# Optimization experiments

Measured on AMD Instinct MI355X. Metric: run time of the kernel, lower is better.

The kernel has to match this reference:

```python
import jax, jax.numpy as jnp
import numpy as np

B, T, H = 2, 1024, 4096
HK, HV, DK, DV = 8, 32, 64, 64
VPK = HV // HK            # value heads per key head = 4
KEY_DIM = HK * DK         # 512
VAL_DIM = HV * DV         # 2048
CONV_DIM = 2 * KEY_DIM + VAL_DIM  # 3072
KSZ = 4
EPS = 1e-5
L2_EPS = 1e-6


def _l2norm(x):
    return x * jax.lax.rsqrt(jnp.sum(x * x, axis=-1, keepdims=True) + L2_EPS)


def setup_inputs() -> dict:
    key = jax.random.key(0)
    ks = jax.random.split(key, 8)
    s = 0.02
    return {
        "hidden_states": jax.random.normal(ks[0], (B, T, H), jnp.float32),
        "W_qkvz": jax.random.normal(ks[1], (H, 2 * KEY_DIM + 2 * VAL_DIM), jnp.float32) * s,
        "W_ba": jax.random.normal(ks[2], (H, 2 * HV), jnp.float32) * s,
        "conv_w": jax.random.normal(ks[3], (CONV_DIM, KSZ), jnp.float32) * 0.1,
        "dt_bias": jnp.ones((HV,), jnp.float32),
        "A_log": jnp.log(jax.random.uniform(ks[4], (HV,), jnp.float32, 1.0, 16.0)),
        "norm_w": jnp.ones((DV,), jnp.float32),
        "W_out": jax.random.normal(ks[5], (VAL_DIM, H), jnp.float32) * s,
    }


def _forward(hidden_states, W_qkvz, W_ba, conv_w, dt_bias, A_log, norm_w, W_out):
    # --- projections ---
    qkvz = hidden_states @ W_qkvz                       # [B,T,5120]
    ba = hidden_states @ W_ba                           # [B,T,64]
    # fix_query_key_value_ordering: per key head [q(Dk), k(Dk), v(vpk*Dv), z(vpk*Dv)]
    qkvz = qkvz.reshape(B, T, HK, 2 * DK + 2 * VPK * DV)
    q = qkvz[..., :DK]                                  # [B,T,HK,DK]
    k = qkvz[..., DK:2 * DK]
    v = qkvz[..., 2 * DK:2 * DK + VPK * DV].reshape(B, T, HV, DV)
    z = qkvz[..., 2 * DK + VPK * DV:].reshape(B, T, HV, DV)
    ba = ba.reshape(B, T, HK, 2 * VPK)
    b = ba[..., :VPK].reshape(B, T, HV)
    a = ba[..., VPK:].reshape(B, T, HV)

    # --- causal depthwise conv over concatenated qkv, then silu ---
    mixed = jnp.concatenate(
        [q.reshape(B, T, KEY_DIM), k.reshape(B, T, KEY_DIM), v.reshape(B, T, VAL_DIM)], axis=-1)
    padded = jnp.pad(mixed, ((0, 0), (KSZ - 1, 0), (0, 0)))
    conv = sum(padded[:, j:j + T, :] * conv_w[:, j] for j in range(KSZ))
    conv = jax.nn.silu(conv)
    q = conv[..., :KEY_DIM].reshape(B, T, HK, DK)
    k = conv[..., KEY_DIM:2 * KEY_DIM].reshape(B, T, HK, DK)
    v = conv[..., 2 * KEY_DIM:].reshape(B, T, HV, DV)

    # --- fused GDN gating: g = -exp(A_log)*softplus(a+dt_bias), beta = sigmoid(b) ---
    g = -jnp.exp(A_log) * jax.nn.softplus(a + dt_bias)  # [B,T,HV]
    beta = jax.nn.sigmoid(b)                            # [B,T,HV]

    # --- q/k l2 norm + scale, broadcast key heads to value heads ---
    q = _l2norm(q) * (DK ** -0.5)
    k = _l2norm(k)
    q = jnp.repeat(q, VPK, axis=2)                      # [B,T,HV,DK]
    k = jnp.repeat(k, VPK, axis=2)

    # --- gated delta-rule recurrence over time ---
    def step(S, inp):
        qt, kt, vt, gt, bt = inp                        # qt/kt [B,HV,DK], vt [B,HV,DV]
        S = S * jnp.exp(gt)[..., None, None]            # decay
        pred = jnp.einsum('bhk,bhkv->bhv', kt, S)
        delta = (vt - pred) * bt[..., None]
        S = S + jnp.einsum('bhk,bhv->bhkv', kt, delta)
        o = jnp.einsum('bhk,bhkv->bhv', qt, S)
        return S, o

    xs = (q.transpose(1, 0, 2, 3), k.transpose(1, 0, 2, 3), v.transpose(1, 0, 2, 3),
          g.transpose(1, 0, 2), beta.transpose(1, 0, 2))
    S0 = jnp.zeros((B, HV, DK, DV), q.dtype)
    _, o = jax.lax.scan(step, S0, xs)                   # [T,B,HV,DV]
    o = o.transpose(1, 0, 2, 3)                         # [B,T,HV,DV]

    # --- gated RMSNorm (norm before gate) + out projection ---
    o_n = o * jax.lax.rsqrt(jnp.mean(o * o, axis=-1, keepdims=True) + EPS) * norm_w
    o_n = o_n * jax.nn.silu(z)
    return o_n.reshape(B, T, VAL_DIM) @ W_out           # [B,T,H]


def reference(hidden_states, W_qkvz, W_ba, conv_w, dt_bias, A_log, norm_w, W_out):
    return _forward(hidden_states, W_qkvz, W_ba, conv_w, dt_bias, A_log, norm_w, W_out)
```

## Files before the change

kernel.cpp:

```cpp
#include <hip/hip_runtime.h>
#include <hip/hip_bf16.h>
#include <cstdint>
#include <cstddef>


typedef __attribute__((ext_vector_type(8))) short short8;
typedef __attribute__((ext_vector_type(4))) float f32x4;

__device__ __forceinline__ short f2bf(float f) {
  union { float f; unsigned u; } x; x.f = f;
  unsigned r = x.u + 0x7fffu + ((x.u >> 16) & 1u);
  return (short)(r >> 16);
}

__device__ __forceinline__ void gl_lds16(const short* g, short* l) {
  __builtin_amdgcn_global_load_lds(
      (const __attribute__((address_space(1))) void*)g,
      (__attribute__((address_space(3))) void*)l, 16, 0, 0);
}

__global__ __launch_bounds__(256) void to_bf16_kernel(const float* __restrict__ x,
                                                      short* __restrict__ y) {
  int i = blockIdx.x * 256 + threadIdx.x;
  float4 v = ((const float4*)x)[i];
  ushort4 r;
  r.x = (unsigned short)f2bf(v.x);
  r.y = (unsigned short)f2bf(v.y);
  r.z = (unsigned short)f2bf(v.z);
  r.w = (unsigned short)f2bf(v.w);
  ((ushort4*)y)[i] = r;
}

__global__ __launch_bounds__(256) void transpose_w1(const float* __restrict__ Wq,
                                                    const float* __restrict__ Wba,
                                                    short* __restrict__ Wt) {
  __shared__ float tile[32][33];
  int n0 = blockIdx.x * 32;
  int k0 = blockIdx.y * 32;
  int t = threadIdx.x;
  int r = t >> 5;
  int c = t & 31;
#pragma unroll
  for (int i = 0; i < 4; ++i) {
    int kl = r + i * 8;
    int n = n0 + c;
    float v = 0.f;
    if (n < 5120) v = Wq[(size_t)(k0 + kl) * 5120 + n];
    else if (n < 5184) v = Wba[(size_t)(k0 + kl) * 64 + (n - 5120)];
    tile[kl][c] = v;
  }
  __syncthreads();
#pragma unroll
  for (int i = 0; i < 4; ++i) {
    int nl = r + i * 8;
    int kl = c;
    Wt[(size_t)(n0 + nl) * 4096 + k0 + kl] = f2bf(tile[kl][nl]);
  }
}

__global__ __launch_bounds__(256) void transpose_w2(const float* __restrict__ W,
                                                    short* __restrict__ Wt) {
  __shared__ float tile[32][33];
  int n0 = blockIdx.x * 32;
  int k0 = blockIdx.y * 32;
  int t = threadIdx.x;
  int r = t >> 5;
  int c = t & 31;
#pragma unroll
  for (int i = 0; i < 4; ++i) {
    int kl = r + i * 8;
    tile[kl][c] = W[(size_t)(k0 + kl) * 4096 + n0 + c];
  }
  __syncthreads();
#pragma unroll
  for (int i = 0; i < 4; ++i) {
    int nl = r + i * 8;
    int kl = c;
    Wt[(size_t)(n0 + nl) * 2048 + k0 + kl] = f2bf(tile[kl][nl]);
  }
}

template <bool GUARD_N>
__global__ __launch_bounds__(256) void gemm128p(const short* __restrict__ A,
                                                const short* __restrict__ Bt,
                                                float* __restrict__ C,
                                                int N, int K, int MT) {
  __shared__ __align__(16) short As[3 * 4096];
  __shared__ __align__(16) short Bs[3 * 4096];
  const int tid = threadIdx.x;
  const int w = tid >> 6, lane = tid & 63;
  const int wm = w >> 1, wn = w & 1;

  const int nwg = gridDim.x;
  const int bid = blockIdx.x;
  const int swz = (bid & 7) * (nwg >> 3) + (bid >> 3);
  const int m0 = (swz % MT) * 128;
  const int n0 = (swz / MT) * 128;

  const int p0 = w * 64 + lane;
  const int rp0 = p0 >> 3, q0 = p0 & 7;
  const int mm0 = q0 ^ (rp0 & 7);
  const int srow = rp0 * 2 + (mm0 >> 2);
  const int scol = (mm0 & 3) << 3;
  const short* Ag = A + (size_t)(m0 + srow) * K + scol;
  const short* Bg = Bt + (size_t)(n0 + srow) * K + scol;
  const size_t rstep = (size_t)64 * K;

  const int fr = lane & 15;
  const int s = lane >> 4;
  int aoff[4], boff[4];
#pragma unroll
  for (int i = 0; i < 4; ++i) {
    int row = wm * 64 + i * 16 + fr;
    int rp = row >> 1;
    int q = (((row & 1) << 2) | s) ^ (rp & 7);
    aoff[i] = (rp * 8 + q) * 8;
  }
#pragma unroll
  for (int j = 0; j < 4; ++j) {
    int row = wn * 64 + j * 16 + fr;
    int rp = row >> 1;
    int q = (((row & 1) << 2) | s) ^ (rp & 7);
    boff[j] = (rp * 8 + q) * 8;
  }

  f32x4 acc[4][4];
#pragma unroll
  for (int i = 0; i < 4; ++i)
#pragma unroll
    for (int j = 0; j < 4; ++j) acc[i][j] = (f32x4){0.f, 0.f, 0.f, 0.f};

  const int NKT = K >> 5;

#define STAGE_A(kt, bb)                                                \
  { const short* g = Ag + (size_t)(kt) * 32;                           \
    gl_lds16(g,         &As[(bb) * 4096 + w * 512]);                   \
    gl_lds16(g + rstep, &As[(bb) * 4096 + 2048 + w * 512]); }
#define STAGE_B(kt, bb)                                                \
  { const short* g = Bg + (size_t)(kt) * 32;                           \
    gl_lds16(g,         &Bs[(bb) * 4096 + w * 512]);                   \
    gl_lds16(g + rstep, &Bs[(bb) * 4096 + 2048 + w * 512]); }

  STAGE_A(0, 0); STAGE_B(0, 0);
  STAGE_A(1, 1); STAGE_B(1, 1);
  asm volatile("s_waitcnt vmcnt(4)" ::: "memory");
  __builtin_amdgcn_s_barrier();
  __builtin_amdgcn_sched_barrier(0);

  int bi = 0;
  for (int kt = 0; kt < NKT; ++kt) {
    int bi2 = bi - 1; if (bi2 < 0) bi2 = 2;
    const short* Ab = &As[bi * 4096];
    const short* Bb = &Bs[bi * 4096];
    short8 af[2], bf[4];
#pragma unroll
    for (int i = 0; i < 2; ++i) af[i] = *(const short8*)&Ab[aoff[i]];
#pragma unroll
    for (int j = 0; j < 4; ++j) bf[j] = *(const short8*)&Bb[boff[j]];
    if (kt + 2 < NKT) STAGE_A(kt + 2, bi2);
    __builtin_amdgcn_s_barrier();
    asm volatile("s_waitcnt lgkmcnt(0)" ::: "memory");
    __builtin_amdgcn_sched_barrier(0);
    __builtin_amdgcn_s_setprio(1);
#pragma unroll
    for (int i = 0; i < 2; ++i)
#pragma unroll
      for (int j = 0; j < 4; ++j)
        acc[i][j] = __builtin_amdgcn_mfma_f32_16x16x32_bf16(af[i], bf[j], acc[i][j], 0, 0, 0);
    __builtin_amdgcn_s_setprio(0);
    __builtin_amdgcn_sched_barrier(0);
#pragma unroll
    for (int i = 0; i < 2; ++i) af[i] = *(const short8*)&Ab[aoff[i + 2]];
    if (kt + 2 < NKT) STAGE_B(kt + 2, bi2);
    if (kt < NKT - 2) { asm volatile("s_waitcnt vmcnt(4)" ::: "memory"); }
    else              { asm volatile("s_waitcnt vmcnt(0)" ::: "memory"); }
    __builtin_amdgcn_s_barrier();
    asm volatile("s_waitcnt lgkmcnt(0)" ::: "memory");
    __builtin_amdgcn_sched_barrier(0);
    __builtin_amdgcn_s_setprio(1);
#pragma unroll
    for (int i = 0; i < 2; ++i)
#pragma unroll
      for (int j = 0; j < 4; ++j)
        acc[i + 2][j] = __builtin_amdgcn_mfma_f32_16x16x32_bf16(af[i], bf[j], acc[i + 2][j], 0, 0, 0);
    __builtin_amdgcn_s_setprio(0);
    __builtin_amdgcn_sched_barrier(0);
    __builtin_amdgcn_s_barrier();
    ++bi; if (bi == 3) bi = 0;
  }
#undef STAGE_A
#undef STAGE_B

  const int rbase = (lane >> 4) << 2;
#pragma unroll
  for (int i = 0; i < 4; ++i) {
#pragma unroll
    for (int j = 0; j < 4; ++j) {
      int col = n0 + wn * 64 + j * 16 + fr;
      if (GUARD_N && col >= N) continue;
      int row = m0 + wm * 64 + i * 16 + rbase;
#pragma unroll
      for (int r = 0; r < 4; ++r)
        C[(size_t)(row + r) * N + col] = acc[i][j][r];
    }
  }
}

__global__ __launch_bounds__(256) void conv_kernel(const float* __restrict__ qkvz,
                                                   const float* __restrict__ conv_w,
                                                   float* __restrict__ mix) {
  __shared__ float sq[1024];
  __shared__ float scale[16];
  int bt = blockIdx.x;
  int t = bt & 1023;
  int tid = threadIdx.x;
  for (int c = tid; c < 3072; c += 256) {
    int col;
    if (c < 512) {
      col = (c >> 6) * 640 + (c & 63);
    } else if (c < 1024) {
      int c2 = c - 512;
      col = (c2 >> 6) * 640 + 64 + (c2 & 63);
    } else {
      int c3 = c - 1024;
      int hv = c3 >> 6;
      col = (hv >> 2) * 640 + 128 + (hv & 3) * 64 + (c3 & 63);
    }
    float acc = 0.f;
#pragma unroll
    for (int j = 0; j < 4; ++j) {
      int tt = t - 3 + j;
      if (tt >= 0) acc += qkvz[(size_t)(bt - 3 + j) * 5184 + col] * conv_w[c * 4 + j];
    }
    float sv = acc / (1.f + __expf(-acc));
    if (c < 1024)
      sq[c] = sv;
    else
      mix[(size_t)bt * 3072 + c] = sv;
  }
  __syncthreads();
  int g = tid >> 4, l = tid & 15;
  float p = 0.f;
#pragma unroll
  for (int i = 0; i < 4; ++i) {
    float v = sq[g * 64 + l * 4 + i];
    p += v * v;
  }
  p += __shfl_xor(p, 1);
  p += __shfl_xor(p, 2);
  p += __shfl_xor(p, 4);
  p += __shfl_xor(p, 8);
  if (l == 0) scale[g] = rsqrtf(p + 1e-6f);
  __syncthreads();
  for (int c = tid; c < 1024; c += 256) {
    float s = scale[c >> 6] * ((c < 512) ? 0.125f : 1.f);
    mix[(size_t)bt * 3072 + c] = sq[c] * s;
  }
}

__global__ __launch_bounds__(256) void gate_kernel(const float* __restrict__ qkvz,
                                                   const float* __restrict__ dt_bias,
                                                   const float* __restrict__ A_log,
                                                   float* __restrict__ gb,
                                                   float* __restrict__ beta) {
  int i = blockIdx.x * 256 + threadIdx.x;
  int hv = i & 31;
  int bt = i >> 5;
  int hk = hv >> 2, vp = hv & 3;
  const float* row = qkvz + (size_t)bt * 5184 + 5120 + hk * 8;
  float bv = row[vp];
  float av = row[4 + vp];
  float x = av + dt_bias[hv];
  float sp = (x > 20.f) ? x : log1pf(expf(x));
  gb[i] = -expf(A_log[hv]) * sp;
  beta[i] = 1.f / (1.f + expf(-bv));
}

__global__ __launch_bounds__(256) void precompute_kernel(
    const float* __restrict__ mix, const float* __restrict__ gbuf,
    const float* __restrict__ betab, float* __restrict__ Wbuf,
    float* __restrict__ Pbuf, float* __restrict__ Rbuf, float* __restrict__ cbuf) {
  __shared__ float Kt[64][68];
  __shared__ float Vb[64][68];
  __shared__ float AM[64][68];
  __shared__ float Mm[64][68];
  __shared__ float Tb[16][17];
  __shared__ float cs[64], bb[64];

  const int u = blockIdx.x;
  const int chunk = u & 15, hv = (u >> 4) & 31, b = u >> 9;
  const int hk = hv >> 2;
  const int t0g = b * 1024 + chunk * 64;
  const int tid = threadIdx.x;
  const int tr = tid >> 2, q4 = tid & 3;

  {
    const float* mrow = mix + (size_t)(t0g + tr) * 3072;
#pragma unroll
    for (int e = 0; e < 4; ++e) {
      int c0 = q4 * 16 + e * 4;
      float4 kv = *(const float4*)(mrow + 512 + hk * 64 + c0);
      Kt[c0 + 0][tr] = kv.x; Kt[c0 + 1][tr] = kv.y;
      Kt[c0 + 2][tr] = kv.z; Kt[c0 + 3][tr] = kv.w;
      *(float4*)&Vb[tr][c0] = *(const float4*)(mrow + 1024 + hv * 64 + c0);
    }
  }
  if (tid < 64) {
    cs[tid] = gbuf[(size_t)(t0g + tid) * 32 + hv];
    bb[tid] = betab[(size_t)(t0g + tid) * 32 + hv];
  }
  __syncthreads();
  for (int off = 1; off < 64; off <<= 1) {
    float v = 0.f;
    if (tid < 64 && tid >= off) v = cs[tid - off];
    __syncthreads();
    if (tid < 64) cs[tid] += v;
    __syncthreads();
  }
  if (tid < 64) cbuf[(size_t)u * 64 + tid] = cs[tid];

  {
    float acc[16];
#pragma unroll
    for (int i = 0; i < 16; ++i) acc[i] = 0.f;
    for (int d = 0; d < 64; ++d) {
      float kv = Kt[d][tr];
#pragma unroll
      for (int e = 0; e < 4; ++e) {
        float4 ks = *(const float4*)&Kt[d][q4 * 16 + e * 4];
        acc[e * 4 + 0] += kv * ks.x; acc[e * 4 + 1] += kv * ks.y;
        acc[e * 4 + 2] += kv * ks.z; acc[e * 4 + 3] += kv * ks.w;
      }
    }
    float bt_ = bb[tr], ct_ = cs[tr];
#pragma unroll
    for (int j = 0; j < 16; ++j) {
      int s = q4 * 16 + j;
      AM[tr][s] = (s < tr) ? bt_ * acc[j] * __expf(ct_ - cs[s]) : 0.f;
    }
  }
  __syncthreads();

  for (int i = tid; i < 64 * 68; i += 256) (&Mm[0][0])[i] = 0.f;
  __syncthreads();
  if (tid < 64) {
    int blk = tid >> 4, j = tid & 15, base = blk * 16;
    Mm[base][base + j] = (j == 0) ? 1.f : 0.f;
    for (int r = 1; r < 16; ++r) {
      float sum = 0.f;
      for (int s = 0; s < r; ++s) sum += AM[base + r][base + s] * Mm[base + s][base + j];
      Mm[base + r][base + j] = ((r == j) ? 1.f : 0.f) - sum;
    }
  }
  __syncthreads();
  for (int d = 1; d < 4; ++d) {
    for (int j = 0; j + d < 4; ++j) {
      int i = j + d;
      int r = tid >> 4, c = tid & 15;
      float tsum = 0.f;
      for (int kb = j; kb < i; ++kb)
        for (int uu = 0; uu < 16; ++uu)
          tsum += AM[i * 16 + r][kb * 16 + uu] * Mm[kb * 16 + uu][j * 16 + c];
      Tb[r][c] = tsum;
      __syncthreads();
      float msum = 0.f;
      for (int uu = 0; uu < 16; ++uu)
        msum += Mm[i * 16 + r][i * 16 + uu] * Tb[uu][c];
      __syncthreads();
      Mm[i * 16 + r][j * 16 + c] = -msum;
      __syncthreads();
    }
  }

  {
    const float* mrow = mix + (size_t)(t0g + tr) * 3072 + hk * 64;
#pragma unroll
    for (int e = 0; e < 4; ++e) {
      int c0 = q4 * 16 + e * 4;
      float4 qv = *(const float4*)(mrow + c0);
      AM[c0 + 0][tr] = qv.x; AM[c0 + 1][tr] = qv.y;
      AM[c0 + 2][tr] = qv.z; AM[c0 + 3][tr] = qv.w;
    }
  }
  __syncthreads();

  {
    float acc[16];
#pragma unroll
    for (int i = 0; i < 16; ++i) acc[i] = 0.f;
    for (int d = 0; d < 64; ++d) {
      float qv = AM[d][tr];
#pragma unroll
      for (int e = 0; e < 4; ++e) {
        float4 ks = *(const float4*)&Kt[d][q4 * 16 + e * 4];
        acc[e * 4 + 0] += qv * ks.x; acc[e * 4 + 1] += qv * ks.y;
        acc[e * 4 + 2] += qv * ks.z; acc[e * 4 + 3] += qv * ks.w;
      }
    }
    float ct_ = cs[tr];
#pragma unroll
    for (int e = 0; e < 4; ++e) {
      int s0 = q4 * 16 + e * 4;
      float4 pv;
      pv.x = (s0 + 0 <= tr) ? acc[e * 4 + 0] * __expf(ct_ - cs[s0 + 0]) : 0.f;
      pv.y = (s0 + 1 <= tr) ? acc[e * 4 + 1] * __expf(ct_ - cs[s0 + 1]) : 0.f;
      pv.z = (s0 + 2 <= tr) ? acc[e * 4 + 2] * __expf(ct_ - cs[s0 + 2]) : 0.f;
      pv.w = (s0 + 3 <= tr) ? acc[e * 4 + 3] * __expf(ct_ - cs[s0 + 3]) : 0.f;
      *(float4*)&Pbuf[(size_t)u * 4096 + tr * 64 + s0] = pv;
    }
  }
  __syncthreads();

  {
    float vals[16];
#pragma unroll
    for (int j = 0; j < 16; ++j) vals[j] = Kt[q4 * 16 + j][tr];
    float sc = bb[tr] * __expf(cs[tr]);
    __syncthreads();
#pragma unroll
    for (int j = 0; j < 16; ++j) Kt[tr][q4 * 16 + j] = vals[j] * sc;
  }
  __syncthreads();

  {
    float acc[16];
#pragma unroll
    for (int i = 0; i < 16; ++i) acc[i] = 0.f;
    for (int s = 0; s < 64; ++s) {
      float m = Mm[tr][s];
#pragma unroll
      for (int e = 0; e < 4; ++e) {
        float4 kk = *(const float4*)&Kt[s][q4 * 16 + e * 4];
        acc[e * 4 + 0] += m * kk.x; acc[e * 4 + 1] += m * kk.y;
        acc[e * 4 + 2] += m * kk.z; acc[e * 4 + 3] += m * kk.w;
      }
    }
#pragma unroll
    for (int e = 0; e < 4; ++e) {
      float4 wv = {acc[e * 4 + 0], acc[e * 4 + 1], acc[e * 4 + 2], acc[e * 4 + 3]};
      *(float4*)&Wbuf[(size_t)u * 4096 + tr * 64 + q4 * 16 + e * 4] = wv;
    }
  }
  {
    float acc[16];
#pragma unroll
    for (int i = 0; i < 16; ++i) acc[i] = 0.f;
    for (int s = 0; s < 64; ++s) {
      float m = Mm[tr][s] * bb[s];
#pragma unroll
      for (int e = 0; e < 4; ++e) {
        float4 vv = *(const float4*)&Vb[s][q4 * 16 + e * 4];
        acc[e * 4 + 0] += m * vv.x; acc[e * 4 + 1] += m * vv.y;
        acc[e * 4 + 2] += m * vv.z; acc[e * 4 + 3] += m * vv.w;
      }
    }
#pragma unroll
    for (int e = 0; e < 4; ++e) {
      float4 rv = {acc[e * 4 + 0], acc[e * 4 + 1], acc[e * 4 + 2], acc[e * 4 + 3]};
      *(float4*)&Rbuf[(size_t)u * 4096 + tr * 64 + q4 * 16 + e * 4] = rv;
    }
  }
}

__global__ __launch_bounds__(1024) void chunk_scan_kernel(
    const float* __restrict__ mix, const float* __restrict__ Wbuf,
    const float* __restrict__ Pbuf, const float* __restrict__ Rbuf,
    const float* __restrict__ cbuf, float* __restrict__ o) {
  __shared__ float Wb[64][68], Pb[64][68], Qh[64][68], Kt[64][68];
  __shared__ float St[16][68], Dt[16][68];
  __shared__ float cs[64];

  const int bid = blockIdx.x;
  const int vs = bid & 3, hv = (bid >> 2) & 31, b = bid >> 7;
  const int hk = hv >> 2;
  const int bh = b * 32 + hv;
  const int ubase = bh * 16;
  const int tid = threadIdx.x;
  const int tr = tid >> 4, cc = tid & 15;

  if (tid < 16 * 68) (&St[0][0])[tid] = 0.f;
  St[cc][tr] = 0.f;

  float4 WN, PN, KN, QN;
  float RN = 0.f, cN = 0.f;
  float e63c = 1.f;

#define ISSUE_LOADS(ch)                                                         \
  {                                                                             \
    size_t uu = (size_t)(ubase + (ch));                                         \
    WN = ((const float4*)(Wbuf + uu * 4096))[tid];                              \
    PN = ((const float4*)(Pbuf + uu * 4096))[tid];                              \
    const float* mrow = mix + (size_t)(b * 1024 + (ch) * 64 + tr) * 3072;       \
    KN = *(const float4*)(mrow + 512 + hk * 64 + cc * 4);                       \
    QN = *(const float4*)(mrow + hk * 64 + cc * 4);                             \
    RN = Rbuf[uu * 4096 + tr * 64 + vs * 16 + cc];                              \
    if (tid < 64) cN = cbuf[uu * 64 + tid];                                     \
  }

#define COMMIT()                                                                \
  {                                                                             \
    *(float4*)&Wb[tr][cc * 4] = WN;                                             \
    *(float4*)&Pb[tr][cc * 4] = PN;                                             \
    if (tid < 64) cs[tid] = cN;                                                 \
    __syncthreads();                                                            \
    float csv = cs[tr], cs63 = cs[63];                                          \
    float sQv = __expf(csv), sKv = __expf(cs63 - csv);                          \
    e63c = __expf(cs63);                                                        \
    float4 qa;                                                                  \
    qa.x = QN.x * sQv; qa.y = QN.y * sQv;                                       \
    qa.z = QN.z * sQv; qa.w = QN.w * sQv;                                       \
    *(float4*)&Qh[tr][cc * 4] = qa;                                             \
    Kt[cc * 4 + 0][tr] = KN.x * sKv;                                            \
    Kt[cc * 4 + 1][tr] = KN.y * sKv;                                            \
    Kt[cc * 4 + 2][tr] = KN.z * sKv;                                            \
    Kt[cc * 4 + 3][tr] = KN.w * sKv;                                            \
  }

  ISSUE_LOADS(0);
  __syncthreads();
  COMMIT();
  float Rv = RN;

  for (int c = 0; c < 16; ++c) {
    if (c < 15) ISSUE_LOADS(c + 1);
    float a0 = 0.f, a1 = 0.f;
#pragma unroll
    for (int k = 0; k < 8; ++k) {
      float4 w4 = *(const float4*)&Wb[tr][k * 4];
      float4 s4 = *(const float4*)&St[cc][k * 4];
      a0 += w4.x * s4.x + w4.y * s4.y + w4.z * s4.z + w4.w * s4.w;
    }
#pragma unroll
    for (int k = 8; k < 16; ++k) {
      float4 w4 = *(const float4*)&Wb[tr][k * 4];
      float4 s4 = *(const float4*)&St[cc][k * 4];
      a1 += w4.x * s4.x + w4.y * s4.y + w4.z * s4.z + w4.w * s4.w;
    }
    Dt[cc][tr] = Rv - a0 - a1;
    __syncthreads();
    {
      float op = 0.f, oq = 0.f, sn = 0.f;
#pragma unroll
      for (int i = 0; i < 16; ++i) {
        float4 p4 = *(const float4*)&Pb[tr][i * 4];
        float4 q4 = *(const float4*)&Qh[tr][i * 4];
        float4 k4 = *(const float4*)&Kt[tr][i * 4];
        float4 d4 = *(const float4*)&Dt[cc][i * 4];
        float4 s4 = *(const float4*)&St[cc][i * 4];
        op += p4.x * d4.x + p4.y * d4.y + p4.z * d4.z + p4.w * d4.w;
        oq += q4.x * s4.x + q4.y * s4.y + q4.z * s4.z + q4.w * s4.w;
        sn += k4.x * d4.x + k4.y * d4.y + k4.z * d4.z + k4.w * d4.w;
      }
      o[((size_t)(bh * 4 + vs) * 1024 + c * 64 + tr) * 16 + cc] = op + oq;
      float snew = St[cc][tr] * e63c + sn;
      __syncthreads();
      St[cc][tr] = snew;
    }
    if (c < 15) {
      COMMIT();
      Rv = RN;
    }
  }
#undef ISSUE_LOADS
#undef COMMIT
}

__global__ __launch_bounds__(256) void rms_gate_kernel(const float* __restrict__ o,
                                                       const float* __restrict__ qkvz,
                                                       const float* __restrict__ norm_w,
                                                       short* __restrict__ on) {
  int bid = blockIdx.x;
  int bh = bid >> 8;
  int tg = bid & 255;
  int b = bh >> 5, hv = bh & 31;
  int t = tg * 4 + (threadIdx.x >> 6);
  int d = threadIdx.x & 63;
  int bt = b * 1024 + t;
  int hk = hv >> 2, vp = hv & 3;
  float x = o[((size_t)(bh * 4 + (d >> 4)) * 1024 + t) * 16 + (d & 15)];
  float ss = x * x;
  ss += __shfl_xor(ss, 1);
  ss += __shfl_xor(ss, 2);
  ss += __shfl_xor(ss, 4);
  ss += __shfl_xor(ss, 8);
  ss += __shfl_xor(ss, 16);
  ss += __shfl_xor(ss, 32);
  float sc = rsqrtf(ss * (1.f / 64.f) + 1e-5f);
  float z = qkvz[(size_t)bt * 5184 + hk * 640 + 384 + vp * 64 + d];
  float val = x * sc * norm_w[d] * (z / (1.f + __expf(-z)));
  on[((size_t)bt * 32 + hv) * 64 + d] = f2bf(val);
}

extern "C" void kernel_launch(void* const* d_in, const int* in_sizes, int n_in,
                              void* d_out, int out_size, void* d_ws, size_t ws_size,
                              hipStream_t stream) {
  const float* hidden = (const float*)d_in[0];
  const float* W_qkvz = (const float*)d_in[1];
  const float* W_ba = (const float*)d_in[2];
  const float* conv_w = (const float*)d_in[3];
  const float* dt_bias = (const float*)d_in[4];
  const float* A_log = (const float*)d_in[5];
  const float* norm_w = (const float*)d_in[6];
  const float* W_out = (const float*)d_in[7];
  float* out = (float*)d_out;

  char* ws = (char*)d_ws;
  short* A_bf = (short*)(ws + 0);
  short* Wt1 = (short*)(ws + 16777216);
  short* Wt2 = (short*)(ws + 59768832);
  float* qkvz = (float*)(ws + 76546048);
  float* mix = (float*)(ws + 119013376);
  float* gbuf = (float*)(ws + 144179200);
  float* beta = (float*)(ws + 144441344);
  float* o = (float*)(ws + 144703488);
  short* on = (short*)(ws + 161480704);
  float* Wbuf = (float*)(ws + 169869312);
  float* Pbuf = (float*)(ws + 186646528);
  float* Rbuf = (float*)(ws + 203423744);
  float* cbuf = (float*)(ws + 220200960);

  to_bf16_kernel<<<8192, 256, 0, stream>>>(hidden, A_bf);
  transpose_w1<<<dim3(164, 128), 256, 0, stream>>>(W_qkvz, W_ba, Wt1);
  transpose_w2<<<dim3(128, 64), 256, 0, stream>>>(W_out, Wt2);
  gemm128p<true><<<656, 256, 0, stream>>>(A_bf, Wt1, qkvz, 5184, 4096, 16);
  conv_kernel<<<2048, 256, 0, stream>>>(qkvz, conv_w, mix);
  gate_kernel<<<256, 256, 0, stream>>>(qkvz, dt_bias, A_log, gbuf, beta);
  precompute_kernel<<<1024, 256, 0, stream>>>(mix, gbuf, beta, Wbuf, Pbuf, Rbuf, cbuf);
  chunk_scan_kernel<<<256, 1024, 0, stream>>>(mix, Wbuf, Pbuf, Rbuf, cbuf, o);
  rms_gate_kernel<<<16384, 256, 0, stream>>>(o, qkvz, norm_w, on);
  gemm128p<false><<<512, 256, 0, stream>>>(on, Wt2, out, 4096, 2048, 16);
}
```

Measured before the change: 564.7 us.

## Fold state-independent chunk products into a precompute pass to shorten the serial scan

Adds a second precompute kernel that multiplies per-chunk P and scaled K matrices against W and R. It produces combined matrices G and H plus intra-chunk output and state contributions. The serial chunk scan then needs only two dot products per step against the state and one barrier round instead of the dependent delta computation. This shortens the latency-bound recurrence, at the cost of an extra kernel launch, more global traffic, and reusing the bf16 input buffer region for H.

```diff
diff --git a/kernel.cpp b/kernel.cpp
--- a/kernel.cpp
+++ b/kernel.cpp
@@ -462,107 +462,184 @@
   }
 }
 
+__global__ __launch_bounds__(256) void precompute2_kernel(
+    const float* __restrict__ mix, const float* __restrict__ cbuf,
+    float* __restrict__ Wbuf, float* __restrict__ Pbuf, float* __restrict__ Rbuf,
+    float* __restrict__ Hbuf) {
+  __shared__ float At[64][132];
+  __shared__ float Bsm[64][188];
+
+  const int u = blockIdx.x;
+  const int chunk = u & 15, hv = (u >> 4) & 31, b = u >> 9;
+  const int hk = hv >> 2;
+  const int t0g = b * 1024 + chunk * 64;
+  const int tid = threadIdx.x;
+  const int tr = tid >> 2, q4 = tid & 3;
+
+  const float c63 = cbuf[(size_t)u * 64 + 63];
+  const float csr = cbuf[(size_t)u * 64 + tr];
+  const float sKv = __expf(c63 - csr);
+
+  {
+    const float* Pr = Pbuf + (size_t)u * 4096 + tr * 64;
+#pragma unroll
+    for (int e = 0; e < 4; ++e) {
+      int k0 = q4 * 16 + e * 4;
+      float4 p4 = *(const float4*)(Pr + k0);
+      At[k0 + 0][tr] = p4.x; At[k0 + 1][tr] = p4.y;
+      At[k0 + 2][tr] = p4.z; At[k0 + 3][tr] = p4.w;
+    }
+    const float* Kr = mix + (size_t)(t0g + tr) * 3072 + 512 + hk * 64;
+#pragma unroll
+    for (int e = 0; e < 4; ++e) {
+      int n = q4 * 16 + e * 4;
+      float4 k4 = *(const float4*)(Kr + n);
+      float4 o4 = {k4.x * sKv, k4.y * sKv, k4.z * sKv, k4.w * sKv};
+      *(float4*)&At[tr][64 + n] = o4;
+    }
+  }
+  {
+    const float* Wr = Wbuf + (size_t)u * 4096 + tr * 64;
+    const float* Rr = Rbuf + (size_t)u * 4096 + tr * 64;
+#pragma unroll
+    for (int e = 0; e < 4; ++e) {
+      int n = q4 * 16 + e * 4;
+      int cp = n + ((n >> 3) << 2);
+      *(float4*)&Bsm[tr][cp] = *(const float4*)(Wr + n);
+      *(float4*)&Bsm[tr][cp + 96] = *(const float4*)(Rr + n);
+    }
+  }
+  __syncthreads();
+
+  const int m0 = (tid >> 4) << 3;
+  const int n0 = (tid & 15) << 3;
+  const int cb = n0 + ((n0 >> 3) << 2);
+  float acc[8][8];
+#pragma unroll
+  for (int i = 0; i < 8; ++i)
+#pragma unroll
+    for (int j = 0; j < 8; ++j) acc[i][j] = 0.f;
+
+  for (int k = 0; k < 64; ++k) {
+    float4 a0 = *(const float4*)&At[k][m0];
+    float4 a1 = *(const float4*)&At[k][m0 + 4];
+    float4 b0 = *(const float4*)&Bsm[k][cb];
+    float4 b1 = *(const float4*)&Bsm[k][cb + 4];
+    float am[8] = {a0.x, a0.y, a0.z, a0.w, a1.x, a1.y, a1.z, a1.w};
+    float bn[8] = {b0.x, b0.y, b0.z, b0.w, b1.x, b1.y, b1.z, b1.w};
+#pragma unroll
+    for (int i = 0; i < 8; ++i)
+#pragma unroll
+      for (int j = 0; j < 8; ++j) acc[i][j] += am[i] * bn[j];
+  }
+
+  if (m0 < 64) {
+    if (n0 < 64) {
+#pragma unroll
+      for (int i = 0; i < 8; ++i) {
+        int t = m0 + i;
+        float ee = __expf(cbuf[(size_t)u * 64 + t]);
+        const float* Qr = mix + (size_t)(t0g + t) * 3072 + hk * 64 + n0;
+        float4 q0 = *(const float4*)(Qr);
+        float4 q1 = *(const float4*)(Qr + 4);
+        float4 g0 = {q0.x * ee - acc[i][0], q0.y * ee - acc[i][1],
+                     q0.z * ee - acc[i][2], q0.w * ee - acc[i][3]};
+        float4 g1 = {q1.x * ee - acc[i][4], q1.y * ee - acc[i][5],
+                     q1.z * ee - acc[i][6], q1.w * ee - acc[i][7]};
+        float* dst = Wbuf + (size_t)u * 4096 + t * 64 + n0;
+        *(float4*)dst = g0; *(float4*)(dst + 4) = g1;
+      }
+    } else {
+#pragma unroll
+      for (int i = 0; i < 8; ++i) {
+        float* dst = Rbuf + (size_t)u * 4096 + (m0 + i) * 64 + (n0 - 64);
+        float4 r0 = {acc[i][0], acc[i][1], acc[i][2], acc[i][3]};
+        float4 r1 = {acc[i][4], acc[i][5], acc[i][6], acc[i][7]};
+        *(float4*)dst = r0; *(float4*)(dst + 4) = r1;
+      }
+    }
+  } else {
+    if (n0 < 64) {
+#pragma unroll
+      for (int i = 0; i < 8; ++i) {
+        float* dst = Hbuf + (size_t)u * 4096 + (m0 - 64 + i) * 64 + n0;
+        float4 h0 = {acc[i][0], acc[i][1], acc[i][2], acc[i][3]};
+        float4 h1 = {acc[i][4], acc[i][5], acc[i][6], acc[i][7]};
+        *(float4*)dst = h0; *(float4*)(dst + 4) = h1;
+      }
+    } else {
+#pragma unroll
+      for (int i = 0; i < 8; ++i) {
+        float* dst = Pbuf + (size_t)u * 4096 + (m0 - 64 + i) * 64 + (n0 - 64);
+        float4 k0v = {acc[i][0], acc[i][1], acc[i][2], acc[i][3]};
+        float4 k1v = {acc[i][4], acc[i][5], acc[i][6], acc[i][7]};
+        *(float4*)dst = k0v; *(float4*)(dst + 4) = k1v;
+      }
+    }
+  }
+}
+
 __global__ __launch_bounds__(1024) void chunk_scan_kernel(
-    const float* __restrict__ mix, const float* __restrict__ Wbuf,
-    const float* __restrict__ Pbuf, const float* __restrict__ Rbuf,
+    const float* __restrict__ Gbuf, const float* __restrict__ Hbuf,
+    const float* __restrict__ ORbuf, const float* __restrict__ KRbuf,
     const float* __restrict__ cbuf, float* __restrict__ o) {
-  __shared__ float Wb[64][68], Pb[64][68], Qh[64][68], Kt[64][68];
-  __shared__ float St[16][68], Dt[16][68];
-  __shared__ float cs[64];
+  __shared__ float Gs[64][72], Hs[64][72];
+  __shared__ float St[16][68];
 
   const int bid = blockIdx.x;
   const int vs = bid & 3, hv = (bid >> 2) & 31, b = bid >> 7;
-  const int hk = hv >> 2;
   const int bh = b * 32 + hv;
   const int ubase = bh * 16;
   const int tid = threadIdx.x;
   const int tr = tid >> 4, cc = tid & 15;
 
-  if (tid < 16 * 68) (&St[0][0])[tid] = 0.f;
-  St[cc][tr] = 0.f;
-
-  float4 WN, PN, KN, QN;
-  float RN = 0.f, cN = 0.f;
-  float e63c = 1.f;
-
-#define ISSUE_LOADS(ch)                                                         \
+  (&St[0][0])[tid] = 0.f;
+  if (tid < 64) (&St[0][0])[1024 + tid] = 0.f;
+
+  float4 GN, HN;
+  float ORn = 0.f, KRn = 0.f, e63n = 0.f;
+
+#define ISSUE(ch)                                                               \
   {                                                                             \
     size_t uu = (size_t)(ubase + (ch));                                         \
-    WN = ((const float4*)(Wbuf + uu * 4096))[tid];                              \
-    PN = ((const float4*)(Pbuf + uu * 4096))[tid];                              \
-    const float* mrow = mix + (size_t)(b * 1024 + (ch) * 64 + tr) * 3072;       \
-    KN = *(const float4*)(mrow + 512 + hk * 64 + cc * 4);                       \
-    QN = *(const float4*)(mrow + hk * 64 + cc * 4);                             \
-    RN = Rbuf[uu * 4096 + tr * 64 + vs * 16 + cc];                              \
-    if (tid < 64) cN = cbuf[uu * 64 + tid];                                     \
-  }
-
-#define COMMIT()                                                                \
-  {                                                                             \
-    *(float4*)&Wb[tr][cc * 4] = WN;                                             \
-    *(float4*)&Pb[tr][cc * 4] = PN;                                             \
-    if (tid < 64) cs[tid] = cN;                                                 \
-    __syncthreads();                                                            \
-    float csv = cs[tr], cs63 = cs[63];                                          \
-    float sQv = __expf(csv), sKv = __expf(cs63 - csv);                          \
-    e63c = __expf(cs63);                                                        \
-    float4 qa;                                                                  \
-    qa.x = QN.x * sQv; qa.y = QN.y * sQv;                                       \
-    qa.z = QN.z * sQv; qa.w = QN.w * sQv;                                       \
-    *(float4*)&Qh[tr][cc * 4] = qa;                                             \
-    Kt[cc * 4 + 0][tr] = KN.x * sKv;                                            \
-    Kt[cc * 4 + 1][tr] = KN.y * sKv;                                            \
-    Kt[cc * 4 + 2][tr] = KN.z * sKv;                                            \
-    Kt[cc * 4 + 3][tr] = KN.w * sKv;                                            \
-  }
-
-  ISSUE_LOADS(0);
-  __syncthreads();
-  COMMIT();
-  float Rv = RN;
+    GN = ((const float4*)(Gbuf + uu * 4096))[tid];                              \
+    HN = ((const float4*)(Hbuf + uu * 4096))[tid];                              \
+    ORn = ORbuf[uu * 4096 + tr * 64 + vs * 16 + cc];                            \
+    KRn = KRbuf[uu * 4096 + tr * 64 + vs * 16 + cc];                            \
+    e63n = cbuf[uu * 64 + 63];                                                  \
+  }
+
+  ISSUE(0);
+  *(float4*)&Gs[tr][cc * 4] = GN;
+  *(float4*)&Hs[tr][cc * 4] = HN;
+  float ORv = ORn, KRv = KRn;
+  float e63 = __expf(e63n);
+  __syncthreads();
 
   for (int c = 0; c < 16; ++c) {
-    if (c < 15) ISSUE_LOADS(c + 1);
-    float a0 = 0.f, a1 = 0.f;
-#pragma unroll
-    for (int k = 0; k < 8; ++k) {
-      float4 w4 = *(const float4*)&Wb[tr][k * 4];
-      float4 s4 = *(const float4*)&St[cc][k * 4];
-      a0 += w4.x * s4.x + w4.y * s4.y + w4.z * s4.z + w4.w * s4.w;
-    }
-#pragma unroll
-    for (int k = 8; k < 16; ++k) {
-      float4 w4 = *(const float4*)&Wb[tr][k * 4];
-      float4 s4 = *(const float4*)&St[cc][k * 4];
-      a1 += w4.x * s4.x + w4.y * s4.y + w4.z * s4.z + w4.w * s4.w;
-    }
-    Dt[cc][tr] = Rv - a0 - a1;
+    if (c < 15) ISSUE(c + 1);
+    float op = ORv, sn = KRv;
+    float sold = St[cc][tr];
+#pragma unroll
+    for (int i = 0; i < 16; ++i) {
+      float4 g4 = *(const float4*)&Gs[tr][i * 4];
+      float4 h4 = *(const float4*)&Hs[tr][i * 4];
+      float4 s4 = *(const float4*)&St[cc][i * 4];
+      op += g4.x * s4.x + g4.y * s4.y + g4.z * s4.z + g4.w * s4.w;
+      sn -= h4.x * s4.x + h4.y * s4.y + h4.z * s4.z + h4.w * s4.w;
+    }
+    o[((size_t)(bh * 4 + vs) * 1024 + c * 64 + tr) * 16 + cc] = op;
+    float snew = sold * e63 + sn;
     __syncthreads();
-    {
-      float op = 0.f, oq = 0.f, sn = 0.f;
-#pragma unroll
-      for (int i = 0; i < 16; ++i) {
-        float4 p4 = *(const float4*)&Pb[tr][i * 4];
-        float4 q4 = *(const float4*)&Qh[tr][i * 4];
-        float4 k4 = *(const float4*)&Kt[tr][i * 4];
-        float4 d4 = *(const float4*)&Dt[cc][i * 4];
-        float4 s4 = *(const float4*)&St[cc][i * 4];
-        op += p4.x * d4.x + p4.y * d4.y + p4.z * d4.z + p4.w * d4.w;
-        oq += q4.x * s4.x + q4.y * s4.y + q4.z * s4.z + q4.w * s4.w;
-        sn += k4.x * d4.x + k4.y * d4.y + k4.z * d4.z + k4.w * d4.w;
-      }
-      o[((size_t)(bh * 4 + vs) * 1024 + c * 64 + tr) * 16 + cc] = op + oq;
-      float snew = St[cc][tr] * e63c + sn;
-      __syncthreads();
-      St[cc][tr] = snew;
-    }
+    St[cc][tr] = snew;
     if (c < 15) {
-      COMMIT();
-      Rv = RN;
-    }
-  }
-#undef ISSUE_LOADS
-#undef COMMIT
+      *(float4*)&Gs[tr][cc * 4] = GN;
+      *(float4*)&Hs[tr][cc * 4] = HN;
+      ORv = ORn; KRv = KRn; e63 = __expf(e63n);
+    }
+    __syncthreads();
+  }
+#undef ISSUE
 }
 
 __global__ __launch_bounds__(256) void rms_gate_kernel(const float* __restrict__ o,
@@ -606,6 +683,7 @@
 
   char* ws = (char*)d_ws;
   short* A_bf = (short*)(ws + 0);
+  float* Hbuf = (float*)(ws + 0);
   short* Wt1 = (short*)(ws + 16777216);
   short* Wt2 = (short*)(ws + 59768832);
   float* qkvz = (float*)(ws + 76546048);
@@ -626,7 +704,8 @@
   conv_kernel<<<2048, 256, 0, stream>>>(qkvz, conv_w, mix);
   gate_kernel<<<256, 256, 0, stream>>>(qkvz, dt_bias, A_log, gbuf, beta);
   precompute_kernel<<<1024, 256, 0, stream>>>(mix, gbuf, beta, Wbuf, Pbuf, Rbuf, cbuf);
-  chunk_scan_kernel<<<256, 1024, 0, stream>>>(mix, Wbuf, Pbuf, Rbuf, cbuf, o);
+  precompute2_kernel<<<1024, 256, 0, stream>>>(mix, cbuf, Wbuf, Pbuf, Rbuf, Hbuf);
+  chunk_scan_kernel<<<256, 1024, 0, stream>>>(Wbuf, Hbuf, Rbuf, Pbuf, cbuf, o);
   rms_gate_kernel<<<16384, 256, 0, stream>>>(o, qkvz, norm_w, on);
   gemm128p<false><<<512, 256, 0, stream>>>(on, Wt2, out, 4096, 2048, 16);
 }
```

New measurement: 529.6 us. -6.2%, faster.
